# Kernel optimization log

Measured on AMD Instinct MI355X. Metric: run time of the kernel, lower is better.

## Reference

```python
import jax, jax.numpy as jnp
import numpy as np

IN_F = 1024
OUT_F = 2048
BATCH = 1024
LAMBD = 0.2
TOL = 1e-4
MAX_ITERS = 100


def setup_inputs() -> dict:
    key = jax.random.key(0)
    kx, kw = jax.random.split(key)
    x = jax.random.normal(kx, (BATCH, IN_F), dtype=jnp.float32)
    # weight init exactly as in torch __init__: randn then column-wise (dim=0) L2 normalization
    w = jax.random.normal(kw, (OUT_F, IN_F), dtype=jnp.float32)
    w = w / jnp.linalg.norm(w, axis=0)  # norm over out_features, broadcast over columns
    A = w.T  # (in, out)
    M = A.T @ A + jnp.eye(OUT_F, dtype=jnp.float32)  # (out, out)
    M_inv = jnp.linalg.inv(M).T
    return {"x": x, "weight": w, "M_inv": M_inv}


def _softshrink(z, lambd):
    return jnp.sign(z) * jnp.maximum(jnp.abs(z) - lambd, 0.0)


def _basis_pursuit_admm(A_dot_b, M_inv, lambd=LAMBD, tol=TOL, max_iters=MAX_ITERS):
    # Mask-based equivalent of the torch dynamic-resizing loop: solved rows are
    # frozen instead of removed; v_solution captures v at the iteration a row converges.
    B, Mdim = A_dot_b.shape
    z = jnp.zeros((B, Mdim), dtype=A_dot_b.dtype)
    solved0 = jnp.zeros((B,), dtype=bool)
    init = (z, z, z, z, solved0)  # v, u, v_prev, v_solution, solved

    def step(carry, _):
        v, u, v_prev, v_sol, solved = carry
        b_eff = A_dot_b + v - u                      # (B, M)
        xk = b_eff @ M_inv                           # (B, M) @ (M, M)
        v_new = _softshrink(xk + u, lambd)
        u_new = u + xk - v_new
        # negligible_improvement on the updated v vs previous v
        dx = jnp.linalg.norm(v_new - v_prev, axis=1)
        xn = jnp.linalg.norm(v_new, axis=1)
        conv = (dx / xn) < tol
        newly = conv & (~solved)
        v_sol = jnp.where(newly[:, None], v_new, v_sol)
        frozen = solved[:, None]
        v = jnp.where(frozen, v, v_new)
        u = jnp.where(frozen, u, u_new)
        solved = solved | newly
        return (v, u, v, v_sol, solved), None

    (v, u, v_prev, v_sol, solved), _ = jax.lax.scan(step, init, None, length=max_iters)
    # Matches torch: rows still unsolved after max_iters keep their initial zero solution.
    return v_sol


def reference(x, weight, M_inv):
    input_shape = x.shape
    b = jax.lax.stop_gradient(x.reshape(x.shape[0], -1))  # x.detach() in torch
    A_dot_b = b @ weight.T                                 # b.matmul(A) with A = weight.T
    encoded = _basis_pursuit_admm(A_dot_b, M_inv)
    decoded = encoded @ weight
    return encoded, decoded.reshape(input_shape)
```

## Files before the change

kernel.cpp:

```cpp
#include <hip/hip_runtime.h>
#include <math.h>

#define BATCH 1024
#define IN_F  1024
#define OUT_F 2048
#define LAMBD 0.2f
#define TOL   1e-4f
#define MAX_ITERS 100

#define KSPLIT 4
#define KCHUNK (OUT_F / KSPLIT)
#define BSCALE 32.0f
#define BSCALE_INV 0.03125f

typedef _Float16 half8 __attribute__((ext_vector_type(8)));
typedef _Float16 half4 __attribute__((ext_vector_type(4)));
typedef float    floatx16 __attribute__((ext_vector_type(16)));
typedef unsigned char fp8_t;

#define GLOAD_LDS16(g, l) __builtin_amdgcn_global_load_lds(              \
    (const __attribute__((address_space(1))) void*)(g),                  \
    (__attribute__((address_space(3))) void*)(l), 16, 0, 0)

__device__ inline int pk4_fp8(float a, float b, float c, float d) {
    int w = __builtin_amdgcn_cvt_pk_fp8_f32(a, b, 0, false);
    w = __builtin_amdgcn_cvt_pk_fp8_f32(c, d, w, true);
    return w;
}
__device__ inline fp8_t enc_fp8(float a) {
    return (fp8_t)(__builtin_amdgcn_cvt_pk_fp8_f32(a, a, 0, false) & 0xff);
}
__device__ inline void cvt4_fp8(int w, float o[4]) {
    o[0] = __builtin_amdgcn_cvt_f32_fp8(w, 0);
    o[1] = __builtin_amdgcn_cvt_f32_fp8(w, 1);
    o[2] = __builtin_amdgcn_cvt_f32_fp8(w, 2);
    o[3] = __builtin_amdgcn_cvt_f32_fp8(w, 3);
}

#define BM 64
#define BN 64
#define BK 16
#define TM 4
#define TN 4
#define LDA (BM + 4)
#define LDB (BN + 4)

__global__ void init_kernel(float4* __restrict__ v16, float4* __restrict__ u16,
                            float4* __restrict__ enc, int* __restrict__ solved) {
    const int i = blockIdx.x * blockDim.x + threadIdx.x;
    const float4 z = make_float4(0.f, 0.f, 0.f, 0.f);
    const int nh = BATCH * OUT_F / 8;
    const int n4 = BATCH * OUT_F / 4;
    if (i < nh) { v16[i] = z; u16[i] = z; }
    if (i < n4) enc[i] = z;
    if (i < BATCH) solved[i] = 0;
}

__global__ __launch_bounds__(256)
void split_b_kernel(const float* __restrict__ B, fp8_t* __restrict__ BhT) {
    __shared__ float tile[32][33];
    const int tid = threadIdx.x;
    const int k0 = blockIdx.y * 32;
    const int n0 = blockIdx.x * 32;
    const int r = tid >> 3;
    const int c4 = (tid & 7) * 4;
    const float4 b4 = *(const float4*)&B[(size_t)(k0 + r) * OUT_F + n0 + c4];
    tile[r][c4 + 0] = b4.x; tile[r][c4 + 1] = b4.y;
    tile[r][c4 + 2] = b4.z; tile[r][c4 + 3] = b4.w;
    __syncthreads();
    const int w = pk4_fp8(tile[c4 + 0][r] * BSCALE, tile[c4 + 1][r] * BSCALE,
                          tile[c4 + 2][r] * BSCALE, tile[c4 + 3][r] * BSCALE);
    *(int*)&BhT[(size_t)(n0 + r) * OUT_F + k0 + c4] = w;
}

__global__ __launch_bounds__(256)
void gemm_nt(const float* __restrict__ A, const float* __restrict__ B,
             _Float16* __restrict__ Abh, fp8_t* __restrict__ Ah,
             int M, int N, int K) {
    __shared__ float As[BK][LDA];
    __shared__ float Bs[BK][LDB];
    const int tid = threadIdx.x;
    const int tx = tid & 15, ty = tid >> 4;
    const int m0 = blockIdx.y * BM;
    const int n0 = blockIdx.x * BN;
    const int lr = tid >> 2;
    const int lk = (tid & 3) * 4;

    float acc[TM][TN] = {};

    for (int k0 = 0; k0 < K; k0 += BK) {
        const float4 a4 = *(const float4*)&A[(size_t)(m0 + lr) * K + k0 + lk];
        const float4 b4 = *(const float4*)&B[(size_t)(n0 + lr) * K + k0 + lk];
        __syncthreads();
        As[lk + 0][lr] = a4.x; As[lk + 1][lr] = a4.y; As[lk + 2][lr] = a4.z; As[lk + 3][lr] = a4.w;
        Bs[lk + 0][lr] = b4.x; Bs[lk + 1][lr] = b4.y; Bs[lk + 2][lr] = b4.z; Bs[lk + 3][lr] = b4.w;
        __syncthreads();
#pragma unroll
        for (int kk = 0; kk < BK; ++kk) {
            const float4 av = *(const float4*)&As[kk][ty * TM];
            const float4 bv = *(const float4*)&Bs[kk][tx * TN];
            const float ar[4] = {av.x, av.y, av.z, av.w};
            const float br[4] = {bv.x, bv.y, bv.z, bv.w};
#pragma unroll
            for (int i = 0; i < TM; ++i)
#pragma unroll
                for (int j = 0; j < TN; ++j)
                    acc[i][j] = fmaf(ar[i], br[j], acc[i][j]);
        }
    }
#pragma unroll
    for (int i = 0; i < TM; ++i) {
        const size_t o = (size_t)(m0 + ty * TM + i) * N + n0 + tx * TN;
        half4 h;
#pragma unroll
        for (int j = 0; j < 4; ++j) h[j] = (_Float16)acc[i][j];
        *(half4*)&Abh[o] = h;
        *(int*)&Ah[o] = pk4_fp8(acc[i][0], acc[i][1], acc[i][2], acc[i][3]);
    }
}

__global__ __launch_bounds__(256)
void xk_mfma(const fp8_t* __restrict__ Ah, const fp8_t* __restrict__ BhT,
             fp8_t* __restrict__ xkp, const int* __restrict__ solved) {
    __shared__ fp8_t sA[128 * 64];
    __shared__ fp8_t sB[128 * 64];
    const int tid = threadIdx.x;
    const int m0 = blockIdx.y * 128;
    const int n0 = blockIdx.x * 128;
    const int kz = blockIdx.z;

    __shared__ int s_active;
    if (tid == 0) s_active = 0;
    __syncthreads();
    if (tid < 128 && solved[m0 + tid] == 0) s_active = 1;
    __syncthreads();
    if (!s_active) return;

    const int wv = tid >> 6;
    const int ln = tid & 63;
    const int half = ln >> 5;
    const int l31 = ln & 31;
    const int wm = (wv >> 1) * 64;
    const int wn = (wv & 1) * 64;

    const int r = tid & 127;
    const int c0 = tid >> 7;
    const fp8_t* gA = Ah  + (size_t)(m0 + r) * OUT_F + kz * KCHUNK;
    const fp8_t* gB = BhT + (size_t)(n0 + r) * OUT_F + kz * KCHUNK;
    fp8_t* lA0 = sA + (c0 * 128 + r) * 16;
    fp8_t* lA1 = sA + ((c0 + 2) * 128 + r) * 16;
    fp8_t* lB0 = sB + (c0 * 128 + r) * 16;
    fp8_t* lB1 = sB + ((c0 + 2) * 128 + r) * 16;

    floatx16 acc[2][2];
#pragma unroll
    for (int a = 0; a < 2; ++a)
#pragma unroll
        for (int b = 0; b < 2; ++b)
#pragma unroll
            for (int q = 0; q < 16; ++q) acc[a][b][q] = 0.f;

    const int ao0 = (wm + l31) * 16 + half * 8;
    const int ao1 = (wm + 32 + l31) * 16 + half * 8;
    const int bo0 = (wn + l31) * 16 + half * 8;
    const int bo1 = (wn + 32 + l31) * 16 + half * 8;

    for (int k = 0; k < KCHUNK; k += 64) {
        __syncthreads();
        GLOAD_LDS16(gA + k + c0 * 16, lA0);
        GLOAD_LDS16(gA + k + (c0 + 2) * 16, lA1);
        GLOAD_LDS16(gB + k + c0 * 16, lB0);
        GLOAD_LDS16(gB + k + (c0 + 2) * 16, lB1);
        __syncthreads();

#pragma unroll
        for (int kk = 0; kk < 4; ++kk) {
            const int cb = kk * 2048;
            const long long a0 = *(const long long*)&sA[cb + ao0];
            const long long a1 = *(const long long*)&sA[cb + ao1];
            const long long b0 = *(const long long*)&sB[cb + bo0];
            const long long b1 = *(const long long*)&sB[cb + bo1];
            acc[0][0] = __builtin_amdgcn_mfma_f32_32x32x16_fp8_fp8(a0, b0, acc[0][0], 0, 0, 0);
            acc[0][1] = __builtin_amdgcn_mfma_f32_32x32x16_fp8_fp8(a0, b1, acc[0][1], 0, 0, 0);
            acc[1][0] = __builtin_amdgcn_mfma_f32_32x32x16_fp8_fp8(a1, b0, acc[1][0], 0, 0, 0);
            acc[1][1] = __builtin_amdgcn_mfma_f32_32x32x16_fp8_fp8(a1, b1, acc[1][1], 0, 0, 0);
        }
    }

    fp8_t* out = xkp + (size_t)kz * BATCH * OUT_F;
#pragma unroll
    for (int mm = 0; mm < 2; ++mm)
#pragma unroll
        for (int nn = 0; nn < 2; ++nn) {
            const int col = n0 + wn + nn * 32 + l31;
#pragma unroll
            for (int q = 0; q < 16; ++q) {
                const int row = m0 + wm + mm * 32 + (q & 3) + 8 * (q >> 2) + 4 * half;
                out[(size_t)row * OUT_F + col] = enc_fp8(acc[mm][nn][q] * BSCALE_INV);
            }
        }
}

__global__ __launch_bounds__(256)
void gemm_nn(const float* __restrict__ A, const float* __restrict__ B,
             float* __restrict__ C, int M, int N, int K) {
    __shared__ float As[BK][LDA];
    __shared__ float Bs[BK][LDB];
    const int tid = threadIdx.x;
    const int tx = tid & 15, ty = tid >> 4;
    const int m0 = blockIdx.y * BM;
    const int n0 = blockIdx.x * BN;
    const int lr = tid >> 2;
    const int lk = (tid & 3) * 4;
    const int kb = tid >> 4;
    const int nb = (tid & 15) * 4;

    float acc[TM][TN] = {};

    for (int k0 = 0; k0 < K; k0 += BK) {
        const float4 a4 = *(const float4*)&A[(size_t)(m0 + lr) * K + k0 + lk];
        const float4 b4 = *(const float4*)&B[(size_t)(k0 + kb) * N + n0 + nb];
        __syncthreads();
        As[lk + 0][lr] = a4.x; As[lk + 1][lr] = a4.y; As[lk + 2][lr] = a4.z; As[lk + 3][lr] = a4.w;
        *(float4*)&Bs[kb][nb] = b4;
        __syncthreads();
#pragma unroll
        for (int kk = 0; kk < BK; ++kk) {
            const float4 av = *(const float4*)&As[kk][ty * TM];
            const float4 bv = *(const float4*)&Bs[kk][tx * TN];
            const float ar[4] = {av.x, av.y, av.z, av.w};
            const float br[4] = {bv.x, bv.y, bv.z, bv.w};
#pragma unroll
            for (int i = 0; i < TM; ++i)
#pragma unroll
                for (int j = 0; j < TN; ++j)
                    acc[i][j] = fmaf(ar[i], br[j], acc[i][j]);
        }
    }
#pragma unroll
    for (int i = 0; i < TM; ++i) {
        float4 o = make_float4(acc[i][0], acc[i][1], acc[i][2], acc[i][3]);
        *(float4*)&C[(size_t)(m0 + ty * TM + i) * N + n0 + tx * TN] = o;
    }
}

__global__ __launch_bounds__(256)
void update_kernel(const fp8_t* __restrict__ xkp, const _Float16* __restrict__ Abh,
                   _Float16* __restrict__ v, _Float16* __restrict__ u,
                   float* __restrict__ enc, fp8_t* __restrict__ Ah,
                   int* __restrict__ solved) {
    const int row = blockIdx.x;
    if (solved[row]) return;
    const int t = threadIdx.x;
    constexpr size_t P = (size_t)BATCH * OUT_F;

    const int c = t * 8;
    const size_t off = (size_t)row * OUT_F + c;
    const int2 q0 = *(const int2*)&xkp[off];
    const int2 q1 = *(const int2*)&xkp[P + off];
    const int2 q2 = *(const int2*)&xkp[2 * P + off];
    const int2 q3 = *(const int2*)&xkp[3 * P + off];
    const half8 u8 = *(const half8*)&u[off];
    const half8 v8 = *(const half8*)&v[off];
    const half8 ab8 = *(const half8*)&Abh[off];

    float f0[4], f1[4], f2[4], f3[4], g0[4], g1[4], g2[4], g3[4];
    cvt4_fp8(q0.x, f0); cvt4_fp8(q1.x, f1); cvt4_fp8(q2.x, f2); cvt4_fp8(q3.x, f3);
    cvt4_fp8(q0.y, g0); cvt4_fp8(q1.y, g1); cvt4_fp8(q2.y, g2); cvt4_fp8(q3.y, g3);
    float xs[8];
#pragma unroll
    for (int j = 0; j < 4; ++j) {
        xs[j] = f0[j] + f1[j] + f2[j] + f3[j];
        xs[j + 4] = g0[j] + g1[j] + g2[j] + g3[j];
    }

    float vn_all[8], ae[8];
    half8 vo, uo;
    float dx2 = 0.f, xn2 = 0.f;
#pragma unroll
    for (int j = 0; j < 8; ++j) {
        const float xk = xs[j];
        const float uv = (float)u8[j];
        const float vp = (float)v8[j];
        const float z = xk + uv;
        const float az = fabsf(z) - LAMBD;
        const float vnew = az > 0.f ? copysignf(az, z) : 0.f;
        const float unew = uv + xk - vnew;
        const float d = vnew - vp;
        dx2 += d * d;
        xn2 += vnew * vnew;
        vn_all[j] = vnew;
        vo[j] = (_Float16)vnew;
        uo[j] = (_Float16)unew;
        ae[j] = (float)ab8[j] + vnew - unew;
    }
    *(half8*)&v[off] = vo;
    *(half8*)&u[off] = uo;
    int2 ah;
    ah.x = pk4_fp8(ae[0], ae[1], ae[2], ae[3]);
    ah.y = pk4_fp8(ae[4], ae[5], ae[6], ae[7]);
    *(int2*)&Ah[off] = ah;

#pragma unroll
    for (int o = 32; o > 0; o >>= 1) {
        dx2 += __shfl_down(dx2, o);
        xn2 += __shfl_down(xn2, o);
    }
    __shared__ float sdx[4], sxn[4];
    __shared__ float s_conv;
    if ((t & 63) == 0) { sdx[t >> 6] = dx2; sxn[t >> 6] = xn2; }
    __syncthreads();
    if (t == 0) {
        const float dxt = sqrtf(sdx[0] + sdx[1] + sdx[2] + sdx[3]);
        const float xnt = sqrtf(sxn[0] + sxn[1] + sxn[2] + sxn[3]);
        const bool conv = (dxt / xnt) < TOL;
        s_conv = conv ? 1.f : 0.f;
        if (conv) solved[row] = 1;
    }
    __syncthreads();
    if (s_conv != 0.f) {
        *(float4*)&enc[off] = make_float4(vn_all[0], vn_all[1], vn_all[2], vn_all[3]);
        *(float4*)&enc[off + 4] = make_float4(vn_all[4], vn_all[5], vn_all[6], vn_all[7]);
    }
}

extern "C" void kernel_launch(void* const* d_in, const int* in_sizes, int n_in,
                              void* d_out, int out_size, void* d_ws, size_t ws_size,
                              hipStream_t stream) {
    (void)in_sizes; (void)n_in; (void)out_size; (void)ws_size;
    const float* x    = (const float*)d_in[0];
    const float* w    = (const float*)d_in[1];
    const float* Minv = (const float*)d_in[2];

    float* enc = (float*)d_out;
    float* dec = enc + (size_t)BATCH * OUT_F;

    constexpr size_t P = (size_t)BATCH * OUT_F;
    _Float16* Abh = (_Float16*)d_ws;
    _Float16* v   = Abh + P;
    _Float16* u   = v + P;
    fp8_t* Ah  = (fp8_t*)(u + P);
    fp8_t* xkp = Ah + P;
    fp8_t* BhT = xkp + 4 * P;
    int* solved = (int*)(BhT + (size_t)OUT_F * OUT_F);

    {
        const int n = BATCH * OUT_F / 4;
        init_kernel<<<(n + 255) / 256, 256, 0, stream>>>(
            (float4*)v, (float4*)u, (float4*)enc, solved);
    }

    split_b_kernel<<<dim3(OUT_F / 32, OUT_F / 32), 256, 0, stream>>>(Minv, BhT);

    gemm_nt<<<dim3(OUT_F / BN, BATCH / BM), 256, 0, stream>>>(x, w, Abh, Ah,
                                                              BATCH, OUT_F, IN_F);

    for (int it = 0; it < MAX_ITERS; ++it) {
        xk_mfma<<<dim3(OUT_F / 128, BATCH / 128, KSPLIT), 256, 0, stream>>>(
            Ah, BhT, xkp, solved);
        update_kernel<<<BATCH, 256, 0, stream>>>(xkp, Abh, v, u, enc, Ah, solved);
    }

    gemm_nn<<<dim3(IN_F / BN, BATCH / BM), 256, 0, stream>>>(enc, w, dec, BATCH, IN_F, OUT_F);
}
```

Measured before the change: 2.412 ms.

## Move prologue and decode GEMMs to f16 MFMA and stage xk outputs via LDS

Replaces the fp32 SIMT GEMMs for A·b and the final decode with f16 MFMA kernels, adding cast and transpose kernels that prepare f16 operands. The xk_mfma epilogue now writes fp8 results into shared memory first and then stores coalesced 16-byte rows instead of scattered byte stores. This targets the fixed-cost GEMMs and the per-iteration store inefficiency. In exchange it adds extra cast launches and workspace, and lowers the decode and A·b precision to f16.

After: 2.282 ms. 1.06x faster.

```diff
diff --git a/kernel.cpp b/kernel.cpp
--- a/kernel.cpp
+++ b/kernel.cpp
@@ -36,14 +36,6 @@
     o[2] = __builtin_amdgcn_cvt_f32_fp8(w, 2);
     o[3] = __builtin_amdgcn_cvt_f32_fp8(w, 3);
 }
-
-#define BM 64
-#define BN 64
-#define BK 16
-#define TM 4
-#define TN 4
-#define LDA (BM + 4)
-#define LDB (BN + 4)
 
 __global__ void init_kernel(float4* __restrict__ v16, float4* __restrict__ u16,
                             float4* __restrict__ enc, int* __restrict__ solved) {
@@ -54,6 +46,36 @@
     if (i < nh) { v16[i] = z; u16[i] = z; }
     if (i < n4) enc[i] = z;
     if (i < BATCH) solved[i] = 0;
+}
+
+__global__ __launch_bounds__(256)
+void cast_f16_kernel(const float* __restrict__ in, _Float16* __restrict__ out, int n) {
+    const int i = (blockIdx.x * 256 + threadIdx.x) * 4;
+    if (i < n) {
+        const float4 f = *(const float4*)&in[i];
+        half4 h;
+        h[0] = (_Float16)f.x; h[1] = (_Float16)f.y;
+        h[2] = (_Float16)f.z; h[3] = (_Float16)f.w;
+        *(half4*)&out[i] = h;
+    }
+}
+
+__global__ __launch_bounds__(256)
+void transpose_w_kernel(const float* __restrict__ W, _Float16* __restrict__ WT) {
+    __shared__ float tile[32][33];
+    const int tid = threadIdx.x;
+    const int row0 = blockIdx.y * 32;
+    const int col0 = blockIdx.x * 32;
+    const int r = tid >> 3;
+    const int c4 = (tid & 7) * 4;
+    const float4 b4 = *(const float4*)&W[(size_t)(row0 + r) * IN_F + col0 + c4];
+    tile[r][c4 + 0] = b4.x; tile[r][c4 + 1] = b4.y;
+    tile[r][c4 + 2] = b4.z; tile[r][c4 + 3] = b4.w;
+    __syncthreads();
+    half4 h;
+#pragma unroll
+    for (int j = 0; j < 4; ++j) h[j] = (_Float16)tile[c4 + j][r];
+    *(half4*)&WT[(size_t)(col0 + r) * OUT_F + row0 + c4] = h;
 }
 
 __global__ __launch_bounds__(256)
@@ -74,60 +96,138 @@
 }
 
 __global__ __launch_bounds__(256)
-void gemm_nt(const float* __restrict__ A, const float* __restrict__ B,
-             _Float16* __restrict__ Abh, fp8_t* __restrict__ Ah,
-             int M, int N, int K) {
-    __shared__ float As[BK][LDA];
-    __shared__ float Bs[BK][LDB];
+void mfma_nt_ab(const _Float16* __restrict__ A, const _Float16* __restrict__ B,
+                _Float16* __restrict__ Abh, fp8_t* __restrict__ Ah,
+                int N, int K) {
+    __shared__ _Float16 sA[128 * 32];
+    __shared__ _Float16 sB[128 * 32];
     const int tid = threadIdx.x;
-    const int tx = tid & 15, ty = tid >> 4;
-    const int m0 = blockIdx.y * BM;
-    const int n0 = blockIdx.x * BN;
-    const int lr = tid >> 2;
-    const int lk = (tid & 3) * 4;
-
-    float acc[TM][TN] = {};
-
-    for (int k0 = 0; k0 < K; k0 += BK) {
-        const float4 a4 = *(const float4*)&A[(size_t)(m0 + lr) * K + k0 + lk];
-        const float4 b4 = *(const float4*)&B[(size_t)(n0 + lr) * K + k0 + lk];
-        __syncthreads();
-        As[lk + 0][lr] = a4.x; As[lk + 1][lr] = a4.y; As[lk + 2][lr] = a4.z; As[lk + 3][lr] = a4.w;
-        Bs[lk + 0][lr] = b4.x; Bs[lk + 1][lr] = b4.y; Bs[lk + 2][lr] = b4.z; Bs[lk + 3][lr] = b4.w;
-        __syncthreads();
-#pragma unroll
-        for (int kk = 0; kk < BK; ++kk) {
-            const float4 av = *(const float4*)&As[kk][ty * TM];
-            const float4 bv = *(const float4*)&Bs[kk][tx * TN];
-            const float ar[4] = {av.x, av.y, av.z, av.w};
-            const float br[4] = {bv.x, bv.y, bv.z, bv.w};
-#pragma unroll
-            for (int i = 0; i < TM; ++i)
-#pragma unroll
-                for (int j = 0; j < TN; ++j)
-                    acc[i][j] = fmaf(ar[i], br[j], acc[i][j]);
-        }
-    }
-#pragma unroll
-    for (int i = 0; i < TM; ++i) {
-        const size_t o = (size_t)(m0 + ty * TM + i) * N + n0 + tx * TN;
-        half4 h;
-#pragma unroll
-        for (int j = 0; j < 4; ++j) h[j] = (_Float16)acc[i][j];
-        *(half4*)&Abh[o] = h;
-        *(int*)&Ah[o] = pk4_fp8(acc[i][0], acc[i][1], acc[i][2], acc[i][3]);
-    }
+    const int m0 = blockIdx.y * 128;
+    const int n0 = blockIdx.x * 128;
+    const int wv = tid >> 6, ln = tid & 63;
+    const int half = ln >> 5, l31 = ln & 31;
+    const int wm = (wv >> 1) * 64, wn = (wv & 1) * 64;
+    const int r0 = tid >> 2, koff = (tid & 3) * 8;
+    const size_t ga0 = (size_t)(m0 + r0) * K + koff;
+    const size_t ga1 = (size_t)(m0 + r0 + 64) * K + koff;
+    const size_t gb0 = (size_t)(n0 + r0) * K + koff;
+    const size_t gb1 = (size_t)(n0 + r0 + 64) * K + koff;
+    const int ldst0 = tid * 8, ldst1 = (256 + tid) * 8;
+
+    floatx16 acc[2][2];
+#pragma unroll
+    for (int a = 0; a < 2; ++a)
+#pragma unroll
+        for (int b = 0; b < 2; ++b)
+#pragma unroll
+            for (int q = 0; q < 16; ++q) acc[a][b][q] = 0.f;
+
+    for (int k = 0; k < K; k += 32) {
+        __syncthreads();
+        GLOAD_LDS16(A + ga0 + k, sA + ldst0);
+        GLOAD_LDS16(A + ga1 + k, sA + ldst1);
+        GLOAD_LDS16(B + gb0 + k, sB + ldst0);
+        GLOAD_LDS16(B + gb1 + k, sB + ldst1);
+        __syncthreads();
+#pragma unroll
+        for (int kk = 0; kk < 2; ++kk) {
+            const int ko = kk * 16 + half * 8;
+            const half8 a0 = *(const half8*)&sA[(wm + l31) * 32 + ko];
+            const half8 a1 = *(const half8*)&sA[(wm + 32 + l31) * 32 + ko];
+            const half8 b0 = *(const half8*)&sB[(wn + l31) * 32 + ko];
+            const half8 b1 = *(const half8*)&sB[(wn + 32 + l31) * 32 + ko];
+            acc[0][0] = __builtin_amdgcn_mfma_f32_32x32x16_f16(a0, b0, acc[0][0], 0, 0, 0);
+            acc[0][1] = __builtin_amdgcn_mfma_f32_32x32x16_f16(a0, b1, acc[0][1], 0, 0, 0);
+            acc[1][0] = __builtin_amdgcn_mfma_f32_32x32x16_f16(a1, b0, acc[1][0], 0, 0, 0);
+            acc[1][1] = __builtin_amdgcn_mfma_f32_32x32x16_f16(a1, b1, acc[1][1], 0, 0, 0);
+        }
+    }
+#pragma unroll
+    for (int mm = 0; mm < 2; ++mm)
+#pragma unroll
+        for (int nn = 0; nn < 2; ++nn) {
+            const int col = n0 + wn + nn * 32 + l31;
+#pragma unroll
+            for (int q = 0; q < 16; ++q) {
+                const int row = m0 + wm + mm * 32 + (q & 3) + 8 * (q >> 2) + 4 * half;
+                const size_t o = (size_t)row * N + col;
+                const float x = acc[mm][nn][q];
+                Abh[o] = (_Float16)x;
+                Ah[o] = enc_fp8(x);
+            }
+        }
+}
+
+__global__ __launch_bounds__(256)
+void mfma_nn_dec(const _Float16* __restrict__ A, const _Float16* __restrict__ B,
+                 float* __restrict__ C, int N, int K) {
+    __shared__ _Float16 sA[128 * 32];
+    __shared__ _Float16 sB[128 * 32];
+    const int tid = threadIdx.x;
+    const int m0 = blockIdx.y * 128;
+    const int n0 = blockIdx.x * 128;
+    const int wv = tid >> 6, ln = tid & 63;
+    const int half = ln >> 5, l31 = ln & 31;
+    const int wm = (wv >> 1) * 64, wn = (wv & 1) * 64;
+    const int r0 = tid >> 2, koff = (tid & 3) * 8;
+    const size_t ga0 = (size_t)(m0 + r0) * K + koff;
+    const size_t ga1 = (size_t)(m0 + r0 + 64) * K + koff;
+    const size_t gb0 = (size_t)(n0 + r0) * K + koff;
+    const size_t gb1 = (size_t)(n0 + r0 + 64) * K + koff;
+    const int ldst0 = tid * 8, ldst1 = (256 + tid) * 8;
+
+    floatx16 acc[2][2];
+#pragma unroll
+    for (int a = 0; a < 2; ++a)
+#pragma unroll
+        for (int b = 0; b < 2; ++b)
+#pragma unroll
+            for (int q = 0; q < 16; ++q) acc[a][b][q] = 0.f;
+
+    for (int k = 0; k < K; k += 32) {
+        __syncthreads();
+        GLOAD_LDS16(A + ga0 + k, sA + ldst0);
+        GLOAD_LDS16(A + ga1 + k, sA + ldst1);
+        GLOAD_LDS16(B + gb0 + k, sB + ldst0);
+        GLOAD_LDS16(B + gb1 + k, sB + ldst1);
+        __syncthreads();
+#pragma unroll
+        for (int kk = 0; kk < 2; ++kk) {
+            const int ko = kk * 16 + half * 8;
+            const half8 a0 = *(const half8*)&sA[(wm + l31) * 32 + ko];
+            const half8 a1 = *(const half8*)&sA[(wm + 32 + l31) * 32 + ko];
+            const half8 b0 = *(const half8*)&sB[(wn + l31) * 32 + ko];
+            const half8 b1 = *(const half8*)&sB[(wn + 32 + l31) * 32 + ko];
+            acc[0][0] = __builtin_amdgcn_mfma_f32_32x32x16_f16(a0, b0, acc[0][0], 0, 0, 0);
+            acc[0][1] = __builtin_amdgcn_mfma_f32_32x32x16_f16(a0, b1, acc[0][1], 0, 0, 0);
+            acc[1][0] = __builtin_amdgcn_mfma_f32_32x32x16_f16(a1, b0, acc[1][0], 0, 0, 0);
+            acc[1][1] = __builtin_amdgcn_mfma_f32_32x32x16_f16(a1, b1, acc[1][1], 0, 0, 0);
+        }
+    }
+#pragma unroll
+    for (int mm = 0; mm < 2; ++mm)
+#pragma unroll
+        for (int nn = 0; nn < 2; ++nn) {
+            const int col = n0 + wn + nn * 32 + l31;
+#pragma unroll
+            for (int q = 0; q < 16; ++q) {
+                const int row = m0 + wm + mm * 32 + (q & 3) + 8 * (q >> 2) + 4 * half;
+                C[(size_t)row * N + col] = acc[mm][nn][q];
+            }
+        }
 }
 
 __global__ __launch_bounds__(256)
 void xk_mfma(const fp8_t* __restrict__ Ah, const fp8_t* __restrict__ BhT,
              fp8_t* __restrict__ xkp, const int* __restrict__ solved) {
-    __shared__ fp8_t sA[128 * 64];
-    __shared__ fp8_t sB[128 * 64];
+    __shared__ fp8_t smem[16384];
+    fp8_t* sA = smem;
+    fp8_t* sB = smem + 8192;
     const int tid = threadIdx.x;
     const int m0 = blockIdx.y * 128;
     const int n0 = blockIdx.x * 128;
     const int kz = blockIdx.z;
+    constexpr size_t P = (size_t)BATCH * OUT_F;
 
     __shared__ int s_active;
     if (tid == 0) s_active = 0;
@@ -187,60 +287,24 @@
         }
     }
 
-    fp8_t* out = xkp + (size_t)kz * BATCH * OUT_F;
+    __syncthreads();
 #pragma unroll
     for (int mm = 0; mm < 2; ++mm)
 #pragma unroll
         for (int nn = 0; nn < 2; ++nn) {
-            const int col = n0 + wn + nn * 32 + l31;
+            const int lcol = wn + nn * 32 + l31;
 #pragma unroll
             for (int q = 0; q < 16; ++q) {
-                const int row = m0 + wm + mm * 32 + (q & 3) + 8 * (q >> 2) + 4 * half;
-                out[(size_t)row * OUT_F + col] = enc_fp8(acc[mm][nn][q] * BSCALE_INV);
+                const int lrow = wm + mm * 32 + (q & 3) + 8 * (q >> 2) + 4 * half;
+                smem[lrow * 128 + lcol] = enc_fp8(acc[mm][nn][q] * BSCALE_INV);
             }
         }
-}
-
-__global__ __launch_bounds__(256)
-void gemm_nn(const float* __restrict__ A, const float* __restrict__ B,
-             float* __restrict__ C, int M, int N, int K) {
-    __shared__ float As[BK][LDA];
-    __shared__ float Bs[BK][LDB];
-    const int tid = threadIdx.x;
-    const int tx = tid & 15, ty = tid >> 4;
-    const int m0 = blockIdx.y * BM;
-    const int n0 = blockIdx.x * BN;
-    const int lr = tid >> 2;
-    const int lk = (tid & 3) * 4;
-    const int kb = tid >> 4;
-    const int nb = (tid & 15) * 4;
-
-    float acc[TM][TN] = {};
-
-    for (int k0 = 0; k0 < K; k0 += BK) {
-        const float4 a4 = *(const float4*)&A[(size_t)(m0 + lr) * K + k0 + lk];
-        const float4 b4 = *(const float4*)&B[(size_t)(k0 + kb) * N + n0 + nb];
-        __syncthreads();
-        As[lk + 0][lr] = a4.x; As[lk + 1][lr] = a4.y; As[lk + 2][lr] = a4.z; As[lk + 3][lr] = a4.w;
-        *(float4*)&Bs[kb][nb] = b4;
-        __syncthreads();
-#pragma unroll
-        for (int kk = 0; kk < BK; ++kk) {
-            const float4 av = *(const float4*)&As[kk][ty * TM];
-            const float4 bv = *(const float4*)&Bs[kk][tx * TN];
-            const float ar[4] = {av.x, av.y, av.z, av.w};
-            const float br[4] = {bv.x, bv.y, bv.z, bv.w};
-#pragma unroll
-            for (int i = 0; i < TM; ++i)
-#pragma unroll
-                for (int j = 0; j < TN; ++j)
-                    acc[i][j] = fmaf(ar[i], br[j], acc[i][j]);
-        }
-    }
-#pragma unroll
-    for (int i = 0; i < TM; ++i) {
-        float4 o = make_float4(acc[i][0], acc[i][1], acc[i][2], acc[i][3]);
-        *(float4*)&C[(size_t)(m0 + ty * TM + i) * N + n0 + tx * TN] = o;
+    __syncthreads();
+    fp8_t* outp = xkp + kz * P + (size_t)m0 * OUT_F + n0;
+#pragma unroll
+    for (int s = 0; s < 4; ++s) {
+        const int f = (s * 256 + tid) * 16;
+        *(int4*)&outp[(size_t)(f >> 7) * OUT_F + (f & 127)] = *(const int4*)&smem[f];
     }
 }
 
@@ -339,7 +403,11 @@
     _Float16* Abh = (_Float16*)d_ws;
     _Float16* v   = Abh + P;
     _Float16* u   = v + P;
-    fp8_t* Ah  = (fp8_t*)(u + P);
+    _Float16* xh  = u + P;
+    _Float16* wh  = xh + (size_t)BATCH * IN_F;
+    _Float16* whT = wh + (size_t)OUT_F * IN_F;
+    _Float16* ench = whT + (size_t)IN_F * OUT_F;
+    fp8_t* Ah  = (fp8_t*)(ench + P);
     fp8_t* xkp = Ah + P;
     fp8_t* BhT = xkp + 4 * P;
     int* solved = (int*)(BhT + (size_t)OUT_F * OUT_F);
@@ -352,8 +420,12 @@
 
     split_b_kernel<<<dim3(OUT_F / 32, OUT_F / 32), 256, 0, stream>>>(Minv, BhT);
 
-    gemm_nt<<<dim3(OUT_F / BN, BATCH / BM), 256, 0, stream>>>(x, w, Abh, Ah,
-                                                              BATCH, OUT_F, IN_F);
+    cast_f16_kernel<<<(BATCH * IN_F / 4 + 255) / 256, 256, 0, stream>>>(x, xh, BATCH * IN_F);
+    cast_f16_kernel<<<(OUT_F * IN_F / 4 + 255) / 256, 256, 0, stream>>>(w, wh, OUT_F * IN_F);
+    transpose_w_kernel<<<dim3(IN_F / 32, OUT_F / 32), 256, 0, stream>>>(w, whT);
+
+    mfma_nt_ab<<<dim3(OUT_F / 128, BATCH / 128), 256, 0, stream>>>(
+        xh, wh, Abh, Ah, OUT_F, IN_F);
 
     for (int it = 0; it < MAX_ITERS; ++it) {
         xk_mfma<<<dim3(OUT_F / 128, BATCH / 128, KSPLIT), 256, 0, stream>>>(
@@ -361,5 +433,7 @@
         update_kernel<<<BATCH, 256, 0, stream>>>(xkp, Abh, v, u, enc, Ah, solved);
     }
 
-    gemm_nn<<<dim3(IN_F / BN, BATCH / BM), 256, 0, stream>>>(enc, w, dec, BATCH, IN_F, OUT_F);
-}
+    cast_f16_kernel<<<(BATCH * OUT_F / 4 + 255) / 256, 256, 0, stream>>>(enc, ench, BATCH * OUT_F);
+    mfma_nn_dec<<<dim3(IN_F / 128, BATCH / 128), 256, 0, stream>>>(
+        ench, whT, dec, IN_F, OUT_F);
+}
```
